# Optimization experiments

Hardware: AMD Instinct MI355X
Metric: run time of the kernel (lower is better)

## Reference

```python
import jax, jax.numpy as jnp
import numpy as np

N_NODES = 50000
N_GRAPHS = 500
BLOCK = N_NODES // N_GRAPHS  # 100 nodes per graph
N_EDGES = 800000
D = 32        # emb_dim = in_feat = out_feat
H = 4         # num_heads
R = 16        # num relations
N_CODES = 20000
L = 2         # n_layers
SLOPE = 0.2
LAM = 0.5     # loop_lambda


def setup_inputs() -> dict:
    key = jax.random.key(0)
    ks = jax.random.split(key, 20)
    node_ids = jax.random.randint(ks[0], (N_NODES,), 0, N_CODES)
    src = jax.random.randint(ks[1], (N_EDGES,), 0, N_NODES)
    # dst must live in the same graph as src (contiguous blocks of BLOCK nodes)
    off = jax.random.randint(ks[2], (N_EDGES,), 0, BLOCK)
    dst = (src // BLOCK) * BLOCK + off
    rel_type = jax.random.randint(ks[3], (N_EDGES,), 0, R)
    node2graph = jnp.repeat(jnp.arange(N_GRAPHS), BLOCK)
    state = jax.random.normal(ks[4], (N_GRAPHS, D), dtype=jnp.float32)
    readout_weight = jax.random.uniform(ks[5], (N_NODES,), dtype=jnp.float32)
    s = 1.0 / np.sqrt(D)
    code_emb = jax.random.uniform(ks[6], (N_CODES, D), minval=-1.0, maxval=1.0)
    rel_table = jax.random.uniform(ks[7], (R, D), minval=-1.0, maxval=1.0)
    W = jax.random.normal(ks[8], (L, R, D, D)) * s       # per-relation weights
    h_bias = jnp.zeros((L, D))
    Wr = jax.random.normal(ks[9], (L, D, H * D)) * s     # fc_rel_att
    br = jnp.zeros((L, H * D))
    We = jax.random.normal(ks[10], (L, D, H * D)) * s    # fc_edge_att
    be = jnp.zeros((L, H * D))
    attn_h = jax.random.normal(ks[11], (L, H, D)) * s
    attn_t = jax.random.normal(ks[12], (L, H, D)) * s
    attn_s = jax.random.normal(ks[13], (L, H, D)) * s
    attn_r = jax.random.normal(ks[14], (L, H, D)) * s
    attn_rs = jax.random.normal(ks[15], (L, H, D)) * s
    return dict(state=state, readout_weight=readout_weight, code_emb=code_emb,
                rel_table=rel_table, W=W, h_bias=h_bias, Wr=Wr, br=br, We=We, be=be,
                attn_h=attn_h, attn_t=attn_t, attn_s=attn_s, attn_r=attn_r, attn_rs=attn_rs,
                node_ids=node_ids, src=src, dst=dst, rel_type=rel_type, node2graph=node2graph)


def _forward(state, readout_weight, code_emb, rel_table, W, h_bias, Wr, br, We, be,
             attn_h, attn_t, attn_s, attn_r, attn_rs, node_ids, src, dst, rel_type, node2graph):
    lrelu = lambda x: jax.nn.leaky_relu(x, SLOPE)
    h = code_emb[node_ids]                      # [N, D]
    N = h.shape[0]
    G = state.shape[0]
    g_src = node2graph[src]                     # [E]
    rel_att = edge_att = None
    for l in range(L):
        # ---- relation attention (cal_rel_att, state path) ----
        rp = (rel_table @ Wr[l] + br[l]).reshape(R, H, D)
        sp = (state @ Wr[l] + br[l]).reshape(G, H, D)
        er = (rp * attn_r[l]).sum(-1)                       # [R, H]
        es = (sp * attn_rs[l]).sum(-1)                      # [G, H]
        ra = jax.nn.softmax(lrelu(er[None, :, :] + es[:, None, :]), axis=1)  # [G, R, H]
        rel_att = ra[g_src, rel_type]                       # [E, H]
        # ---- edge attention (cal_edge_att, state path) ----
        hp = (h @ We[l] + be[l]).reshape(N, H, D)           # multi-head src feat
        eh = (hp * attn_h[l]).sum(-1)                       # [N, H]
        et = (hp * attn_t[l]).sum(-1)                       # [N, H]
        nsp = (state[node2graph] @ We[l] + be[l]).reshape(N, H, D)
        esn = (nsp * attn_s[l]).sum(-1)                     # [N, H]
        e = lrelu(esn[src] + eh[src] + et[dst])             # [E, H]
        emax = jax.ops.segment_max(e, dst, num_segments=N)
        ex = jnp.exp(e - emax[dst])
        den = jax.ops.segment_sum(ex, dst, num_segments=N)
        edge_att = ex / den[dst]                            # edge_softmax over dst
        # ---- per-relation message: matmul(h_src, W[etype]) ----
        # transform all nodes per relation, then gather (same math as per-edge bmm)
        hW = jnp.einsum('nhd,rde->rnhe', hp, W[l])          # [R, N, H, D]
        msg = hW[rel_type, src]                             # [E, H, D]
        msg = (msg * edge_att[..., None] * rel_att[..., None]).sum(axis=1)  # [E, D]
        agg = jax.ops.segment_sum(msg, dst, num_segments=N) + h_bias[l]
        h = jax.nn.relu((1.0 - LAM) * agg + LAM * h)        # self-loop blend + relu
    x = jax.ops.segment_sum(h * readout_weight[:, None], node2graph, num_segments=G)
    return x, rel_att, edge_att


def reference(state, readout_weight, code_emb, rel_table, W, h_bias, Wr, br, We, be,
              attn_h, attn_t, attn_s, attn_r, attn_rs, node_ids, src, dst, rel_type, node2graph):
    return _forward(state, readout_weight, code_emb, rel_table, W, h_bias, Wr, br, We, be,
                    attn_h, attn_t, attn_s, attn_r, attn_rs, node_ids, src, dst, rel_type, node2graph)
```

## Files before the change

### kernel.cpp

```cpp
#include <hip/hip_runtime.h>
#include <hip/hip_fp16.h>

#define DI __device__ __forceinline__

constexpr int NGRAPH = 500;
constexpr int EDGES  = 800000;
constexpr int NNODE  = 50000;
constexpr int CAP    = 64;
constexpr int SCAT_BLOCKS = (EDGES + 255) / 256;

constexpr size_t WI_CURS  = 0;
constexpr size_t WI_SMETA = 50048;
constexpr size_t WF_PREP  = WI_SMETA + (size_t)NNODE * CAP;
constexpr size_t WF_WFRAG = WF_PREP + 672;
constexpr size_t WH_WC    = WF_WFRAG + 20480;

constexpr int S_H    = 0;
constexpr int S_HP   = 8000;
constexpr int S_U    = 33600;
constexpr int S_EH   = 136800;
constexpr int S_ET   = 138400;
constexpr int S_DEN  = 140000;
constexpr int S_RA   = 141600;
constexpr int S_ESG  = 141856;
constexpr int S_AH   = 141872;
constexpr int S_AT   = 142384;
constexpr int S_MLDS = 142896;
constexpr int S_RP   = 151088;
constexpr int S_TOTAL = 151496;
constexpr int UROW = 516;

typedef _Float16 f16x8 __attribute__((ext_vector_type(8)));
typedef _Float16 f16x2 __attribute__((ext_vector_type(2)));
typedef float f32x4 __attribute__((ext_vector_type(4)));

DI float lrelu(float x) { return x >= 0.f ? x : 0.2f * x; }
DI f16x8 u4_to_f16x8(uint4 u) { f16x8 r; __builtin_memcpy(&r, &u, 16); return r; }
DI f16x8 two_u2(uint2 a, uint2 b) { return u4_to_f16x8(make_uint4(a.x, a.y, b.x, b.y)); }
DI float h2f(unsigned short u) { __half hv; __builtin_memcpy(&hv, &u, 2); return __half2float(hv); }

DI float fdot2u(unsigned a, unsigned b, float c) {
    f16x2 av, bv;
    __builtin_memcpy(&av, &a, 4);
    __builtin_memcpy(&bv, &b, 4);
    return __builtin_amdgcn_fdot2(av, bv, c, false);
}

DI int hpIdx(int n, int c) { return n * 128 + (c ^ ((n & 7) << 3)); }

__global__ void k_prep(const int* __restrict__ src, const int* __restrict__ dst,
                       const int* __restrict__ rt, int* __restrict__ curs,
                       int* __restrict__ smeta,
                       const float* __restrict__ rel_table, const float* __restrict__ Wr,
                       const float* __restrict__ br, const float* __restrict__ We,
                       const float* __restrict__ be, const float* __restrict__ attn_r,
                       const float* __restrict__ attn_rs, const float* __restrict__ attn_s,
                       const float* __restrict__ W, float* __restrict__ prep,
                       uint4* __restrict__ wf) {
    __shared__ float wra[2][32][4];
    __shared__ float sbias[2][3][4];
    int bb = blockIdx.x, t = threadIdx.x;
    if (bb < SCAT_BLOCKS) {
        int e = bb * 256 + t;
        if (e >= EDGES) return;
        int s = src[e], d = dst[e], r = rt[e];
        int g = (unsigned)d / 100u;
        int pos = atomicAdd(&curs[d], 1);
        if (pos < CAP)
            smeta[((size_t)d << 6) + pos] = (s - g * 100) | (r << 7) | (e << 11);
        return;
    }
    int b = bb - SCAT_BLOCKS;
    if (b == 0) {
        {
            int l = t >> 7, k = (t >> 2) & 31, h = t & 3;
            float a = 0.f, b2 = 0.f, c = 0.f;
            for (int d2 = 0; d2 < 32; ++d2) {
                float w1 = Wr[(size_t)(l*32 + k)*128 + h*32 + d2];
                float w2 = We[(size_t)(l*32 + k)*128 + h*32 + d2];
                a  += w1 * attn_r [l*128 + h*32 + d2];
                b2 += w1 * attn_rs[l*128 + h*32 + d2];
                c  += w2 * attn_s [l*128 + h*32 + d2];
            }
            wra[l][k][h] = a;
            prep[128 + (l*32 + k)*4 + h] = b2;
            prep[384 + (l*32 + k)*4 + h] = c;
        }
        if (t < 24) {
            int l = t / 12, which = (t % 12) / 4, h = t % 4;
            const float* bp = (which == 2) ? be : br;
            const float* ap = (which == 0) ? attn_r : (which == 1 ? attn_rs : attn_s);
            float s = 0.f;
            for (int d2 = 0; d2 < 32; ++d2) s += bp[l*128 + h*32 + d2] * ap[l*128 + h*32 + d2];
            sbias[l][which][h] = s;
        }
        __syncthreads();
        if (t < 128) {
            int l = t >> 6, r = (t >> 2) & 15, h = t & 3;
            float s = sbias[l][0][h];
            for (int k = 0; k < 32; ++k) s += rel_table[r*32 + k] * wra[l][k][h];
            prep[(l*16 + r)*4 + h] = s;
        }
        if (t < 8) {
            int l = t >> 2, h = t & 3;
            prep[640 + l*4 + h] = sbias[l][1][h];
            prep[648 + l*4 + h] = sbias[l][2][h];
        }
    } else if (b <= 16) {
        int fi = (b - 1) * 256 + t;
        int ln = fi & 63, Nt = (fi >> 6) & 1, rel = (fi >> 7) & 15, l = fi >> 11;
        int j = Nt*16 + (ln & 15), k0 = (ln >> 4) << 3;
        unsigned short fr[8];
        #pragma unroll
        for (int i = 0; i < 8; ++i) {
            __half hv = __float2half(W[(((size_t)l*16 + rel)*32 + k0 + i)*32 + j]);
            __builtin_memcpy(&fr[i], &hv, 2);
        }
        uint4 o;
        o.x = fr[0] | ((unsigned)fr[1] << 16);
        o.y = fr[2] | ((unsigned)fr[3] << 16);
        o.z = fr[4] | ((unsigned)fr[5] << 16);
        o.w = fr[6] | ((unsigned)fr[7] << 16);
        wf[fi] = o;
    } else {
        int fi = (b - 17) * 256 + t;
        int ln = fi & 63, Nt = (fi >> 6) & 7, l = fi >> 9;
        int c = Nt*16 + (ln & 15);
        int phys = (c & 3)*32 + (c >> 2);
        int k0 = (ln >> 4) << 3;
        unsigned short fr[8];
        #pragma unroll
        for (int i = 0; i < 8; ++i) {
            __half hv = __float2half(We[(size_t)l*4096 + (k0 + i)*128 + phys]);
            __builtin_memcpy(&fr[i], &hv, 2);
        }
        uint4 o;
        o.x = fr[0] | ((unsigned)fr[1] << 16);
        o.y = fr[2] | ((unsigned)fr[3] << 16);
        o.z = fr[4] | ((unsigned)fr[5] << 16);
        o.w = fr[6] | ((unsigned)fr[7] << 16);
        wf[4096 + fi] = o;
    }
}

__global__ void __launch_bounds__(1024, 1)
k_fused(const float* __restrict__ state, const float* __restrict__ rw,
        const float* __restrict__ code_emb, const float* __restrict__ h_bias,
        const float* __restrict__ be, const float* __restrict__ attn_h,
        const float* __restrict__ attn_t, const int* __restrict__ node_ids,
        const int* __restrict__ curs, const int* __restrict__ smeta,
        const float* __restrict__ prep, const uint4* __restrict__ wf,
        unsigned short* __restrict__ wc,
        float* __restrict__ xout, float* __restrict__ relOut, float* __restrict__ edgeOut) {
    extern __shared__ char smem[];
    __half* hH  = (__half*)(smem + S_H);
    __half* hpH = (__half*)(smem + S_HP);
    __half* Uh  = (__half*)(smem + S_U);
    float* ehp  = (float*)(smem + S_EH);
    float* etp  = (float*)(smem + S_ET);
    float* denp = (float*)(smem + S_DEN);
    float* rap  = (float*)(smem + S_RA);
    float* esgp = (float*)(smem + S_ESG);
    float* sAH  = (float*)(smem + S_AH);
    float* sAT  = (float*)(smem + S_AT);
    int*   mlds = (int*)(smem + S_MLDS);
    int*   rp   = (int*)(smem + S_RP);
    const uint4* wfe = wf + 4096;

    const int g = blockIdx.x;
    const int t = threadIdx.x;
    const int lane = t & 63, w = t >> 6;
    const int ln15 = lane & 15, q = lane >> 4, q8 = q << 3;
    const int MtA = w % 7, NtA = w / 7;
    const bool hasT = (w < 14);
    const int cg = w >> 1;
    const int colc = cg * 16 + ln15;
    const int physc = (colc & 3) * 32 + (colc >> 2);
    const int Mt0 = (w & 1) ? 4 : 0;
    const int Mt1 = (w & 1) ? 7 : 4;

    unsigned short* wcg = wc + ((size_t)g << 13);
    const uint2* wcu = (const uint2*)wcg;

    for (int i = t; i < 1600; i += 1024) {
        int n = i >> 4, dp = i & 15;
        int id = node_ids[g * 100 + n];
        float2 v = *(const float2*)&code_emb[(size_t)id * 32 + dp * 2];
        *(__half2*)&hH[n * 40 + dp * 2] = __floats2half2_rn(v.x, v.y);
    }
    if (t < 100) { int c = curs[g * 100 + t]; rp[t + 1] = c < CAP ? c : CAP; }
    if (t == 0) rp[0] = 0;
    __syncthreads();
    for (int o = 1; o < 128; o <<= 1) {
        int v = 0;
        if (t <= 100 && t >= o) v = rp[t - o];
        __syncthreads();
        if (t <= 100 && t >= o) rp[t] += v;
        __syncthreads();
    }
    for (int i = t; i < 100 * CAP; i += 1024) {
        int bin = i >> 6, pos = i & 63;
        int lo = rp[bin], cnt = rp[bin + 1] - lo;
        if (pos < cnt)
            mlds[lo + pos] = smeta[(((size_t)(g * 100 + bin)) << 6) + pos];
    }

    for (int l = 0; l < 2; ++l) {
        __syncthreads();

        for (int i = t; i < 6450; i += 1024) ((uint4*)(smem + S_U))[i] = make_uint4(0, 0, 0, 0);
        if (t < 128) {
            sAH[t] = attn_h[l * 128 + (t & 3) * 32 + (t >> 2)];
            sAT[t] = attn_t[l * 128 + (t & 3) * 32 + (t >> 2)];
        }
        {
            uint4 bwe = wfe[(l * 8 + cg) * 64 + lane];
            f16x8 bw = u4_to_f16x8(bwe);
            float beC = be[l * 128 + physc];
            f32x4 z = {0.f, 0.f, 0.f, 0.f};
            for (int Mt = Mt0; Mt < Mt1; ++Mt) {
                const __half* hr = hH + (Mt * 16 + ln15) * 40 + q8;
                f32x4 pc = __builtin_amdgcn_mfma_f32_16x16x32_f16(
                    two_u2(*(const uint2*)hr, *(const uint2*)(hr + 4)), bw, z, 0, 0, 0);
                #pragma unroll
                for (int i = 0; i < 4; ++i) {
                    int n = Mt * 16 + q * 4 + i;
                    if (n < 100) hpH[hpIdx(n, colc)] = __float2half(pc[i] + beC);
                }
            }
        }
        {
            int k32 = lane & 31;
            float sG = state[g * 32 + k32];
            float4 frs = *(const float4*)&prep[128 + l * 128 + k32 * 4];
            float4 fes = *(const float4*)&prep[384 + l * 128 + k32 * 4];
            float p0 = sG * frs.x, p1 = sG * frs.y, p2 = sG * frs.z, p3 = sG * frs.w;
            float q0 = sG * fes.x, q1 = sG * fes.y, q2 = sG * fes.z, q3 = sG * fes.w;
            #pragma unroll
            for (int m = 1; m < 32; m <<= 1) {
                p0 += __shfl_xor(p0, m); p1 += __shfl_xor(p1, m);
                p2 += __shfl_xor(p2, m); p3 += __shfl_xor(p3, m);
                q0 += __shfl_xor(q0, m); q1 += __shfl_xor(q1, m);
                q2 += __shfl_xor(q2, m); q3 += __shfl_xor(q3, m);
            }
            int h = lane & 3;
            float esh  = (h & 2) ? ((h & 1) ? p3 : p2) : ((h & 1) ? p1 : p0);
            float esgh = (h & 2) ? ((h & 1) ? q3 : q2) : ((h & 1) ? q1 : q0);
            esh  += prep[640 + l * 4 + h];
            esgh += prep[648 + l * 4 + h];
            if (lane < 4) esgp[lane] = esgh;
            float er = prep[l * 64 + lane];
            float ex = __expf(lrelu(er + esh));
            float s = ex;
            s += __shfl_xor(s, 4); s += __shfl_xor(s, 8);
            s += __shfl_xor(s, 16); s += __shfl_xor(s, 32);
            rap[lane] = ex / s;
        }
        __syncthreads();

        if (t < 100) {
            int s = t;
            int sw = (s & 7) << 3;
            float eh[4] = {0, 0, 0, 0}, et[4] = {0, 0, 0, 0};
            #pragma unroll 4
            for (int i = 0; i < 16; ++i) {
                uint4 hv = *(const uint4*)&hpH[s * 128 + ((i * 8) ^ sw)];
                unsigned short hu[8];
                __builtin_memcpy(hu, &hv, 16);
                #pragma unroll
                for (int k = 0; k < 8; ++k) {
                    float f = h2f(hu[k]);
                    eh[k & 3] += f * sAH[i * 8 + k];
                    et[k & 3] += f * sAT[i * 8 + k];
                }
            }
            *(float4*)&ehp[s * 4] = make_float4(eh[0], eh[1], eh[2], eh[3]);
            *(float4*)&etp[s * 4] = make_float4(et[0], et[1], et[2], et[3]);
        }
        __syncthreads();

        if (t < 400) {
            int d = t >> 2, h = t & 3;
            int lo = rp[d], hi = rp[d + 1];
            float etd = etp[d * 4 + h] + esgp[h];
            float den = 0.f;
            for (int e = lo; e < hi; ++e) {
                int m = mlds[e];
                den += __expf(lrelu(ehp[(m & 127) * 4 + h] + etd));
            }
            denp[d * 4 + h] = den;
            float inv = 1.f / den;
            bool wAtt = (l == 1);
            for (int e = lo; e < hi; ++e) {
                int m = mlds[e];
                int r = (m >> 7) & 15;
                float a = __expf(lrelu(ehp[(m & 127) * 4 + h] + etd)) * inv;
                __half ch = __float2half(a * rap[r * 4 + h]);
                __builtin_memcpy(&wcg[e * 4 + h], &ch, 2);
                if (wAtt) {
                    int oe = (m >> 11) & 0xFFFFF;
                    edgeOut[(size_t)oe * 4 + h] = a;
                    relOut[(size_t)oe * 4 + h] = rap[r * 4 + h];
                }
            }
        }
        __syncthreads();

        if (t < 800) {
            int d = t >> 3, j = t & 7;
            int lo = rp[d], hi = rp[d + 1];
            for (int e = lo; e < hi; ++e) {
                int m = mlds[e];
                int s = m & 127, r = (m >> 7) & 15;
                uint2 cc = wcu[e];
                int sw = (s & 7) << 3;
                uint4 hv0 = *(const uint4*)&hpH[s * 128 + ((j * 16) ^ sw)];
                uint4 hv1 = *(const uint4*)&hpH[s * 128 + ((j * 16 + 8) ^ sw)];
                float v0 = fdot2u(cc.x, hv0.x, fdot2u(cc.y, hv0.y, 0.f));
                float v1 = fdot2u(cc.x, hv0.z, fdot2u(cc.y, hv0.w, 0.f));
                float v2 = fdot2u(cc.x, hv1.x, fdot2u(cc.y, hv1.y, 0.f));
                float v3 = fdot2u(cc.x, hv1.z, fdot2u(cc.y, hv1.w, 0.f));
                __half2 v01 = __floats2half2_rn(v0, v1);
                __half2 v23 = __floats2half2_rn(v2, v3);
                __half2* up = (__half2*)(Uh + d * UROW + r * 32 + j * 4);
                up[0] = __hadd2(up[0], v01);
                up[1] = __hadd2(up[1], v23);
            }
        }
        __syncthreads();

        f32x4 accA = {0.f, 0.f, 0.f, 0.f};
        if (hasT) {
            #pragma unroll 4
            for (int rel = 0; rel < 16; ++rel) {
                uint4 bAu = wf[((l * 16 + rel) * 2 + NtA) * 64 + lane];
                const __half* up = Uh + (MtA * 16 + ln15) * UROW + rel * 32 + q8;
                f16x8 af = two_u2(*(const uint2*)up, *(const uint2*)(up + 4));
                accA = __builtin_amdgcn_mfma_f32_16x16x32_f16(af, u4_to_f16x8(bAu), accA, 0, 0, 0);
            }
        }
        if (hasT) {
            int dcol = NtA * 16 + ln15;
            float bias = h_bias[l * 32 + dcol];
            #pragma unroll
            for (int i = 0; i < 4; ++i) {
                int n = MtA * 16 + q * 4 + i;
                if (n < 100) {
                    float hold = __half2float(hH[n * 40 + dcol]);
                    float hn = fmaxf(0.f, 0.5f * (accA[i] + bias) + 0.5f * hold);
                    hH[n * 40 + dcol] = __float2half(hn);
                }
            }
        }
    }
    __syncthreads();

    float* redp = (float*)(smem + S_U);
    {
        int part = t >> 5, d = t & 31;
        float acc = 0.f;
        for (int n = part; n < 100; n += 32)
            acc += __half2float(hH[n * 40 + d]) * rw[g * 100 + n];
        redp[part * 32 + d] = acc;
    }
    __syncthreads();
    if (t < 32) {
        float s = 0.f;
        #pragma unroll
        for (int p = 0; p < 32; ++p) s += redp[p * 32 + t];
        xout[g * 32 + t] = s;
    }
}

extern "C" void kernel_launch(void* const* d_in, const int* in_sizes, int n_in,
                              void* d_out, int out_size, void* d_ws, size_t ws_size,
                              hipStream_t stream) {
    const float* state     = (const float*)d_in[0];
    const float* rw        = (const float*)d_in[1];
    const float* code_emb  = (const float*)d_in[2];
    const float* rel_table = (const float*)d_in[3];
    const float* W         = (const float*)d_in[4];
    const float* h_bias    = (const float*)d_in[5];
    const float* Wr        = (const float*)d_in[6];
    const float* br        = (const float*)d_in[7];
    const float* We        = (const float*)d_in[8];
    const float* be        = (const float*)d_in[9];
    const float* attn_h    = (const float*)d_in[10];
    const float* attn_t    = (const float*)d_in[11];
    const float* attn_s    = (const float*)d_in[12];
    const float* attn_r    = (const float*)d_in[13];
    const float* attn_rs   = (const float*)d_in[14];
    const int* node_ids    = (const int*)d_in[15];
    const int* src         = (const int*)d_in[16];
    const int* dst         = (const int*)d_in[17];
    const int* rtype       = (const int*)d_in[18];

    float* out = (float*)d_out;
    float* xout = out;
    float* relOut = out + (size_t)NGRAPH * 32;
    float* edgeOut = relOut + (size_t)EDGES * 4;

    int* wsi = (int*)d_ws;
    float* wsf = (float*)d_ws;
    int* curs   = wsi + WI_CURS;
    int* smeta  = wsi + WI_SMETA;
    float* prep = wsf + WF_PREP;
    uint4* wfrag = (uint4*)(wsf + WF_WFRAG);
    unsigned short* wc = (unsigned short*)(wsf + WH_WC);

    (void)hipMemsetAsync(curs, 0, NNODE * sizeof(int), stream);
    k_prep<<<SCAT_BLOCKS + 21, 256, 0, stream>>>(src, dst, rtype, curs, smeta,
                                                 rel_table, Wr, br, We, be,
                                                 attn_r, attn_rs, attn_s, W, prep, wfrag);

    (void)hipFuncSetAttribute((const void*)k_fused, hipFuncAttributeMaxDynamicSharedMemorySize, S_TOTAL);
    k_fused<<<NGRAPH, 1024, S_TOTAL, stream>>>(state, rw, code_emb, h_bias, be,
                                               attn_h, attn_t, node_ids, curs, smeta,
                                               prep, wfrag, wc, xout, relOut, edgeOut);
}
```

Baseline: 169.0 us.

## Split edge-softmax denominator across more threads, cache exps, prefetch aggregation loop

Adds a separate phase where 800 threads each compute half of a destination/head edge range, storing unnormalised exponentials as fp16 in the per-graph coefficient buffer and partial denominators in shared memory. The normalisation phase then reads those cached values instead of recomputing exp twice. The attention-logit dot products switch to packed half2 FMAs with fp16 attention vectors. The message-aggregation loop software-prefetches the next edge's metadata and features. This costs an extra barrier and fp16 accumulation precision in the logits and stored exponentials.

```diff
diff --git a/kernel.cpp b/kernel.cpp
--- a/kernel.cpp
+++ b/kernel.cpp
@@ -20,14 +20,14 @@
 constexpr int S_U    = 33600;
 constexpr int S_EH   = 136800;
 constexpr int S_ET   = 138400;
-constexpr int S_DEN  = 140000;
 constexpr int S_RA   = 141600;
 constexpr int S_ESG  = 141856;
 constexpr int S_AH   = 141872;
 constexpr int S_AT   = 142384;
 constexpr int S_MLDS = 142896;
 constexpr int S_RP   = 151088;
-constexpr int S_TOTAL = 151496;
+constexpr int S_DEN2 = 151496;
+constexpr int S_TOTAL = S_DEN2 + 3200;
 constexpr int UROW = 516;
 
 typedef _Float16 f16x8 __attribute__((ext_vector_type(8)));
@@ -158,13 +158,13 @@
     __half* Uh  = (__half*)(smem + S_U);
     float* ehp  = (float*)(smem + S_EH);
     float* etp  = (float*)(smem + S_ET);
-    float* denp = (float*)(smem + S_DEN);
     float* rap  = (float*)(smem + S_RA);
     float* esgp = (float*)(smem + S_ESG);
-    float* sAH  = (float*)(smem + S_AH);
-    float* sAT  = (float*)(smem + S_AT);
+    __half* sAHh = (__half*)(smem + S_AH);
+    __half* sATh = (__half*)(smem + S_AT);
     int*   mlds = (int*)(smem + S_MLDS);
     int*   rp   = (int*)(smem + S_RP);
+    float* den2 = (float*)(smem + S_DEN2);
     const uint4* wfe = wf + 4096;
 
     const int g = blockIdx.x;
@@ -210,8 +210,8 @@
 
         for (int i = t; i < 6450; i += 1024) ((uint4*)(smem + S_U))[i] = make_uint4(0, 0, 0, 0);
         if (t < 128) {
-            sAH[t] = attn_h[l * 128 + (t & 3) * 32 + (t >> 2)];
-            sAT[t] = attn_t[l * 128 + (t & 3) * 32 + (t >> 2)];
+            sAHh[t] = __float2half(attn_h[l * 128 + (t & 3) * 32 + (t >> 2)]);
+            sATh[t] = __float2half(attn_t[l * 128 + (t & 3) * 32 + (t >> 2)]);
         }
         {
             uint4 bwe = wfe[(l * 8 + cg) * 64 + lane];
@@ -259,47 +259,68 @@
         __syncthreads();
 
         if (t < 100) {
-            int s = t;
-            int sw = (s & 7) << 3;
-            float eh[4] = {0, 0, 0, 0}, et[4] = {0, 0, 0, 0};
-            #pragma unroll 4
+            int s = t, sw = (s & 7) << 3;
+            __half2 eh01 = __floats2half2_rn(0.f, 0.f), eh23 = eh01;
+            __half2 et01 = eh01, et23 = eh01;
+            const __half2* ahp = (const __half2*)sAHh;
+            const __half2* atp = (const __half2*)sATh;
+            #pragma unroll
             for (int i = 0; i < 16; ++i) {
                 uint4 hv = *(const uint4*)&hpH[s * 128 + ((i * 8) ^ sw)];
-                unsigned short hu[8];
-                __builtin_memcpy(hu, &hv, 16);
-                #pragma unroll
-                for (int k = 0; k < 8; ++k) {
-                    float f = h2f(hu[k]);
-                    eh[k & 3] += f * sAH[i * 8 + k];
-                    et[k & 3] += f * sAT[i * 8 + k];
-                }
-            }
-            *(float4*)&ehp[s * 4] = make_float4(eh[0], eh[1], eh[2], eh[3]);
-            *(float4*)&etp[s * 4] = make_float4(et[0], et[1], et[2], et[3]);
+                __half2 a01 = *(__half2*)&hv.x, a23 = *(__half2*)&hv.y;
+                __half2 b01 = *(__half2*)&hv.z, b23 = *(__half2*)&hv.w;
+                eh01 = __hfma2(a01, ahp[i * 4 + 0], eh01);
+                eh23 = __hfma2(a23, ahp[i * 4 + 1], eh23);
+                eh01 = __hfma2(b01, ahp[i * 4 + 2], eh01);
+                eh23 = __hfma2(b23, ahp[i * 4 + 3], eh23);
+                et01 = __hfma2(a01, atp[i * 4 + 0], et01);
+                et23 = __hfma2(a23, atp[i * 4 + 1], et23);
+                et01 = __hfma2(b01, atp[i * 4 + 2], et01);
+                et23 = __hfma2(b23, atp[i * 4 + 3], et23);
+            }
+            float2 f01 = __half22float2(eh01), f23 = __half22float2(eh23);
+            *(float4*)&ehp[s * 4] = make_float4(f01.x, f01.y, f23.x, f23.y);
+            float2 g01 = __half22float2(et01), g23 = __half22float2(et23);
+            *(float4*)&etp[s * 4] = make_float4(g01.x, g01.y, g23.x, g23.y);
+        }
+        __syncthreads();
+
+        if (t < 800) {
+            int d = t >> 3, h = (t >> 1) & 3, half = t & 1;
+            int lo0 = rp[d], hi0 = rp[d + 1];
+            int mid = (lo0 + hi0 + 1) >> 1;
+            int lo = half ? mid : lo0, hi = half ? hi0 : mid;
+            float etd = etp[d * 4 + h] + esgp[h];
+            float den = 0.f;
+            int m = (lo < hi) ? mlds[lo] : 0;
+            float ev = (lo < hi) ? ehp[(m & 127) * 4 + h] : 0.f;
+            for (int e = lo; e < hi; ++e) {
+                int m2 = 0; float ev2 = 0.f;
+                if (e + 1 < hi) { m2 = mlds[e + 1]; ev2 = ehp[(m2 & 127) * 4 + h]; }
+                float x = __expf(lrelu(ev + etd));
+                __half ch = __float2half(x);
+                __builtin_memcpy(&wcg[e * 4 + h], &ch, 2);
+                den += x;
+                m = m2; ev = ev2;
+            }
+            den2[t] = den;
         }
         __syncthreads();
 
         if (t < 400) {
             int d = t >> 2, h = t & 3;
             int lo = rp[d], hi = rp[d + 1];
-            float etd = etp[d * 4 + h] + esgp[h];
-            float den = 0.f;
-            for (int e = lo; e < hi; ++e) {
-                int m = mlds[e];
-                den += __expf(lrelu(ehp[(m & 127) * 4 + h] + etd));
-            }
-            denp[d * 4 + h] = den;
+            float den = den2[d * 8 + h * 2] + den2[d * 8 + h * 2 + 1];
             float inv = 1.f / den;
-            bool wAtt = (l == 1);
             for (int e = lo; e < hi; ++e) {
                 int m = mlds[e];
                 int r = (m >> 7) & 15;
-                float a = __expf(lrelu(ehp[(m & 127) * 4 + h] + etd)) * inv;
-                __half ch = __float2half(a * rap[r * 4 + h]);
+                float x = h2f(wcg[e * 4 + h]) * inv;
+                __half ch = __float2half(x * rap[r * 4 + h]);
                 __builtin_memcpy(&wcg[e * 4 + h], &ch, 2);
-                if (wAtt) {
+                if (l == 1) {
                     int oe = (m >> 11) & 0xFFFFF;
-                    edgeOut[(size_t)oe * 4 + h] = a;
+                    edgeOut[(size_t)oe * 4 + h] = x;
                     relOut[(size_t)oe * 4 + h] = rap[r * 4 + h];
                 }
             }
@@ -309,22 +330,35 @@
         if (t < 800) {
             int d = t >> 3, j = t & 7;
             int lo = rp[d], hi = rp[d + 1];
-            for (int e = lo; e < hi; ++e) {
-                int m = mlds[e];
-                int s = m & 127, r = (m >> 7) & 15;
-                uint2 cc = wcu[e];
-                int sw = (s & 7) << 3;
-                uint4 hv0 = *(const uint4*)&hpH[s * 128 + ((j * 16) ^ sw)];
-                uint4 hv1 = *(const uint4*)&hpH[s * 128 + ((j * 16 + 8) ^ sw)];
-                float v0 = fdot2u(cc.x, hv0.x, fdot2u(cc.y, hv0.y, 0.f));
-                float v1 = fdot2u(cc.x, hv0.z, fdot2u(cc.y, hv0.w, 0.f));
-                float v2 = fdot2u(cc.x, hv1.x, fdot2u(cc.y, hv1.y, 0.f));
-                float v3 = fdot2u(cc.x, hv1.z, fdot2u(cc.y, hv1.w, 0.f));
-                __half2 v01 = __floats2half2_rn(v0, v1);
-                __half2 v23 = __floats2half2_rn(v2, v3);
-                __half2* up = (__half2*)(Uh + d * UROW + r * 32 + j * 4);
-                up[0] = __hadd2(up[0], v01);
-                up[1] = __hadd2(up[1], v23);
+            if (lo < hi) {
+                int m = mlds[lo];
+                uint2 cc = wcu[lo];
+                int s0 = m & 127, sw0 = (s0 & 7) << 3;
+                uint4 hv0 = *(const uint4*)&hpH[s0 * 128 + ((j * 16) ^ sw0)];
+                uint4 hv1 = *(const uint4*)&hpH[s0 * 128 + ((j * 16 + 8) ^ sw0)];
+                for (int e = lo; e < hi; ++e) {
+                    int m2 = 0;
+                    uint2 cc2 = make_uint2(0, 0);
+                    uint4 nv0 = make_uint4(0, 0, 0, 0), nv1 = nv0;
+                    if (e + 1 < hi) {
+                        m2 = mlds[e + 1];
+                        cc2 = wcu[e + 1];
+                        int s2 = m2 & 127, sw2 = (s2 & 7) << 3;
+                        nv0 = *(const uint4*)&hpH[s2 * 128 + ((j * 16) ^ sw2)];
+                        nv1 = *(const uint4*)&hpH[s2 * 128 + ((j * 16 + 8) ^ sw2)];
+                    }
+                    int r = (m >> 7) & 15;
+                    float v0 = fdot2u(cc.x, hv0.x, fdot2u(cc.y, hv0.y, 0.f));
+                    float v1 = fdot2u(cc.x, hv0.z, fdot2u(cc.y, hv0.w, 0.f));
+                    float v2 = fdot2u(cc.x, hv1.x, fdot2u(cc.y, hv1.y, 0.f));
+                    float v3 = fdot2u(cc.x, hv1.z, fdot2u(cc.y, hv1.w, 0.f));
+                    __half2 v01 = __floats2half2_rn(v0, v1);
+                    __half2 v23 = __floats2half2_rn(v2, v3);
+                    __half2* up = (__half2*)(Uh + d * UROW + r * 32 + j * 4);
+                    up[0] = __hadd2(up[0], v01);
+                    up[1] = __hadd2(up[1], v23);
+                    m = m2; cc = cc2; hv0 = nv0; hv1 = nv1;
+                }
             }
         }
         __syncthreads();
```

Result: slower. 175.1 us (+3.6%).

## Split relation scatter into four passes to shrink LDS and raise occupancy

Applied to the files above, without the earlier changes.

The per-graph U buffer now holds only 4 relations at a time instead of 16, so the relation loop runs in four passes of scatter then MFMA. This cuts LDS from about 151KB to about 72KB and halves the block size to 512 threads, so more than one block can sit on a CU. Waves pick up a second MFMA tile, and the attention vectors are stored as half. The cost is four scans over each node's edge list with skipped edges, plus extra barriers and zeroing per pass, and less parallelism inside each block.

```diff
diff --git a/kernel.cpp b/kernel.cpp
--- a/kernel.cpp
+++ b/kernel.cpp
@@ -18,17 +18,16 @@
 constexpr int S_H    = 0;
 constexpr int S_HP   = 8000;
 constexpr int S_U    = 33600;
-constexpr int S_EH   = 136800;
-constexpr int S_ET   = 138400;
-constexpr int S_DEN  = 140000;
-constexpr int S_RA   = 141600;
-constexpr int S_ESG  = 141856;
-constexpr int S_AH   = 141872;
-constexpr int S_AT   = 142384;
-constexpr int S_MLDS = 142896;
-constexpr int S_RP   = 151088;
-constexpr int S_TOTAL = 151496;
-constexpr int UROW = 516;
+constexpr int S_EH   = 60000;
+constexpr int S_ET   = 61600;
+constexpr int S_RA   = 63200;
+constexpr int S_ESG  = 63456;
+constexpr int S_AH   = 63472;
+constexpr int S_AT   = 63728;
+constexpr int S_MLDS = 63984;
+constexpr int S_RP   = 72176;
+constexpr int S_TOTAL = 72584;
+constexpr int UROW = 132;
 
 typedef _Float16 f16x8 __attribute__((ext_vector_type(8)));
 typedef _Float16 f16x2 __attribute__((ext_vector_type(2)));
@@ -143,7 +142,7 @@
     }
 }
 
-__global__ void __launch_bounds__(1024, 1)
+__global__ void __launch_bounds__(512, 4)
 k_fused(const float* __restrict__ state, const float* __restrict__ rw,
         const float* __restrict__ code_emb, const float* __restrict__ h_bias,
         const float* __restrict__ be, const float* __restrict__ attn_h,
@@ -158,11 +157,10 @@
     __half* Uh  = (__half*)(smem + S_U);
     float* ehp  = (float*)(smem + S_EH);
     float* etp  = (float*)(smem + S_ET);
-    float* denp = (float*)(smem + S_DEN);
     float* rap  = (float*)(smem + S_RA);
     float* esgp = (float*)(smem + S_ESG);
-    float* sAH  = (float*)(smem + S_AH);
-    float* sAT  = (float*)(smem + S_AT);
+    __half* sAHh = (__half*)(smem + S_AH);
+    __half* sATh = (__half*)(smem + S_AT);
     int*   mlds = (int*)(smem + S_MLDS);
     int*   rp   = (int*)(smem + S_RP);
     const uint4* wfe = wf + 4096;
@@ -172,17 +170,15 @@
     const int lane = t & 63, w = t >> 6;
     const int ln15 = lane & 15, q = lane >> 4, q8 = q << 3;
     const int MtA = w % 7, NtA = w / 7;
-    const bool hasT = (w < 14);
-    const int cg = w >> 1;
-    const int colc = cg * 16 + ln15;
+    const int MtB = (w + 8) % 7, NtB = (w + 8) / 7;
+    const bool hasB = (w < 6);
+    const int colc = w * 16 + ln15;
     const int physc = (colc & 3) * 32 + (colc >> 2);
-    const int Mt0 = (w & 1) ? 4 : 0;
-    const int Mt1 = (w & 1) ? 7 : 4;
 
     unsigned short* wcg = wc + ((size_t)g << 13);
     const uint2* wcu = (const uint2*)wcg;
 
-    for (int i = t; i < 1600; i += 1024) {
+    for (int i = t; i < 1600; i += 512) {
         int n = i >> 4, dp = i & 15;
         int id = node_ids[g * 100 + n];
         float2 v = *(const float2*)&code_emb[(size_t)id * 32 + dp * 2];
@@ -198,7 +194,7 @@
         if (t <= 100 && t >= o) rp[t] += v;
         __syncthreads();
     }
-    for (int i = t; i < 100 * CAP; i += 1024) {
+    for (int i = t; i < 100 * CAP; i += 512) {
         int bin = i >> 6, pos = i & 63;
         int lo = rp[bin], cnt = rp[bin + 1] - lo;
         if (pos < cnt)
@@ -208,17 +204,16 @@
     for (int l = 0; l < 2; ++l) {
         __syncthreads();
 
-        for (int i = t; i < 6450; i += 1024) ((uint4*)(smem + S_U))[i] = make_uint4(0, 0, 0, 0);
         if (t < 128) {
-            sAH[t] = attn_h[l * 128 + (t & 3) * 32 + (t >> 2)];
-            sAT[t] = attn_t[l * 128 + (t & 3) * 32 + (t >> 2)];
+            sAHh[t] = __float2half(attn_h[l * 128 + (t & 3) * 32 + (t >> 2)]);
+            sATh[t] = __float2half(attn_t[l * 128 + (t & 3) * 32 + (t >> 2)]);
         }
         {
-            uint4 bwe = wfe[(l * 8 + cg) * 64 + lane];
+            uint4 bwe = wfe[(l * 8 + w) * 64 + lane];
             f16x8 bw = u4_to_f16x8(bwe);
             float beC = be[l * 128 + physc];
             f32x4 z = {0.f, 0.f, 0.f, 0.f};
-            for (int Mt = Mt0; Mt < Mt1; ++Mt) {
+            for (int Mt = 0; Mt < 7; ++Mt) {
                 const __half* hr = hH + (Mt * 16 + ln15) * 40 + q8;
                 f32x4 pc = __builtin_amdgcn_mfma_f32_16x16x32_f16(
                     two_u2(*(const uint2*)hr, *(const uint2*)(hr + 4)), bw, z, 0, 0, 0);
@@ -270,8 +265,8 @@
                 #pragma unroll
                 for (int k = 0; k < 8; ++k) {
                     float f = h2f(hu[k]);
-                    eh[k & 3] += f * sAH[i * 8 + k];
-                    et[k & 3] += f * sAT[i * 8 + k];
+                    eh[k & 3] += f * __half2float(sAHh[i * 8 + k]);
+                    et[k & 3] += f * __half2float(sATh[i * 8 + k]);
                 }
             }
             *(float4*)&ehp[s * 4] = make_float4(eh[0], eh[1], eh[2], eh[3]);
@@ -288,7 +283,6 @@
                 int m = mlds[e];
                 den += __expf(lrelu(ehp[(m & 127) * 4 + h] + etd));
             }
-            denp[d * 4 + h] = den;
             float inv = 1.f / den;
             bool wAtt = (l == 1);
             for (int e = lo; e < hi; ++e) {
@@ -306,40 +300,63 @@
         }
         __syncthreads();
 
-        if (t < 800) {
-            int d = t >> 3, j = t & 7;
-            int lo = rp[d], hi = rp[d + 1];
-            for (int e = lo; e < hi; ++e) {
-                int m = mlds[e];
-                int s = m & 127, r = (m >> 7) & 15;
-                uint2 cc = wcu[e];
-                int sw = (s & 7) << 3;
-                uint4 hv0 = *(const uint4*)&hpH[s * 128 + ((j * 16) ^ sw)];
-                uint4 hv1 = *(const uint4*)&hpH[s * 128 + ((j * 16 + 8) ^ sw)];
-                float v0 = fdot2u(cc.x, hv0.x, fdot2u(cc.y, hv0.y, 0.f));
-                float v1 = fdot2u(cc.x, hv0.z, fdot2u(cc.y, hv0.w, 0.f));
-                float v2 = fdot2u(cc.x, hv1.x, fdot2u(cc.y, hv1.y, 0.f));
-                float v3 = fdot2u(cc.x, hv1.z, fdot2u(cc.y, hv1.w, 0.f));
-                __half2 v01 = __floats2half2_rn(v0, v1);
-                __half2 v23 = __floats2half2_rn(v2, v3);
-                __half2* up = (__half2*)(Uh + d * UROW + r * 32 + j * 4);
-                up[0] = __hadd2(up[0], v01);
-                up[1] = __hadd2(up[1], v23);
-            }
-        }
-        __syncthreads();
-
         f32x4 accA = {0.f, 0.f, 0.f, 0.f};
-        if (hasT) {
-            #pragma unroll 4
-            for (int rel = 0; rel < 16; ++rel) {
-                uint4 bAu = wf[((l * 16 + rel) * 2 + NtA) * 64 + lane];
-                const __half* up = Uh + (MtA * 16 + ln15) * UROW + rel * 32 + q8;
-                f16x8 af = two_u2(*(const uint2*)up, *(const uint2*)(up + 4));
-                accA = __builtin_amdgcn_mfma_f32_16x16x32_f16(af, u4_to_f16x8(bAu), accA, 0, 0, 0);
-            }
-        }
-        if (hasT) {
+        f32x4 accB = {0.f, 0.f, 0.f, 0.f};
+        for (int p = 0; p < 4; ++p) {
+            for (int i = t; i < 1650; i += 512) ((uint4*)(smem + S_U))[i] = make_uint4(0, 0, 0, 0);
+            __syncthreads();
+
+            if (t < 400) {
+                int d = t >> 2, j = t & 3;
+                int lo = rp[d], hi = rp[d + 1];
+                for (int e = lo; e < hi; ++e) {
+                    int m = mlds[e];
+                    int r = (m >> 7) & 15;
+                    if ((r >> 2) != p) continue;
+                    int s = m & 127;
+                    uint2 cc = wcu[e];
+                    int sw = (s & 7) << 3;
+                    uint4 hv0 = *(const uint4*)&hpH[s * 128 + ((j * 32) ^ sw)];
+                    uint4 hv1 = *(const uint4*)&hpH[s * 128 + ((j * 32 + 8) ^ sw)];
+                    uint4 hv2 = *(const uint4*)&hpH[s * 128 + ((j * 32 + 16) ^ sw)];
+                    uint4 hv3 = *(const uint4*)&hpH[s * 128 + ((j * 32 + 24) ^ sw)];
+                    float v0 = fdot2u(cc.x, hv0.x, fdot2u(cc.y, hv0.y, 0.f));
+                    float v1 = fdot2u(cc.x, hv0.z, fdot2u(cc.y, hv0.w, 0.f));
+                    float v2 = fdot2u(cc.x, hv1.x, fdot2u(cc.y, hv1.y, 0.f));
+                    float v3 = fdot2u(cc.x, hv1.z, fdot2u(cc.y, hv1.w, 0.f));
+                    float v4 = fdot2u(cc.x, hv2.x, fdot2u(cc.y, hv2.y, 0.f));
+                    float v5 = fdot2u(cc.x, hv2.z, fdot2u(cc.y, hv2.w, 0.f));
+                    float v6 = fdot2u(cc.x, hv3.x, fdot2u(cc.y, hv3.y, 0.f));
+                    float v7 = fdot2u(cc.x, hv3.z, fdot2u(cc.y, hv3.w, 0.f));
+                    __half2* up = (__half2*)(Uh + d * UROW + (r & 3) * 32 + j * 8);
+                    up[0] = __hadd2(up[0], __floats2half2_rn(v0, v1));
+                    up[1] = __hadd2(up[1], __floats2half2_rn(v2, v3));
+                    up[2] = __hadd2(up[2], __floats2half2_rn(v4, v5));
+                    up[3] = __hadd2(up[3], __floats2half2_rn(v6, v7));
+                }
+            }
+            __syncthreads();
+
+            #pragma unroll
+            for (int kq = 0; kq < 4; ++kq) {
+                int rel = p * 4 + kq;
+                {
+                    uint4 bAu = wf[((l * 16 + rel) * 2 + NtA) * 64 + lane];
+                    const __half* up = Uh + (MtA * 16 + ln15) * UROW + kq * 32 + q8;
+                    f16x8 af = two_u2(*(const uint2*)up, *(const uint2*)(up + 4));
+                    accA = __builtin_amdgcn_mfma_f32_16x16x32_f16(af, u4_to_f16x8(bAu), accA, 0, 0, 0);
+                }
+                if (hasB) {
+                    uint4 bBu = wf[((l * 16 + rel) * 2 + NtB) * 64 + lane];
+                    const __half* up = Uh + (MtB * 16 + ln15) * UROW + kq * 32 + q8;
+                    f16x8 af = two_u2(*(const uint2*)up, *(const uint2*)(up + 4));
+                    accB = __builtin_amdgcn_mfma_f32_16x16x32_f16(af, u4_to_f16x8(bBu), accB, 0, 0, 0);
+                }
+            }
+            __syncthreads();
+        }
+
+        {
             int dcol = NtA * 16 + ln15;
             float bias = h_bias[l * 32 + dcol];
             #pragma unroll
@@ -352,6 +369,19 @@
                 }
             }
         }
+        if (hasB) {
+            int dcol = NtB * 16 + ln15;
+            float bias = h_bias[l * 32 + dcol];
+            #pragma unroll
+            for (int i = 0; i < 4; ++i) {
+                int n = MtB * 16 + q * 4 + i;
+                if (n < 100) {
+                    float hold = __half2float(hH[n * 40 + dcol]);
+                    float hn = fmaxf(0.f, 0.5f * (accB[i] + bias) + 0.5f * hold);
+                    hH[n * 40 + dcol] = __float2half(hn);
+                }
+            }
+        }
     }
     __syncthreads();
 
@@ -359,7 +389,7 @@
     {
         int part = t >> 5, d = t & 31;
         float acc = 0.f;
-        for (int n = part; n < 100; n += 32)
+        for (int n = part; n < 100; n += 16)
             acc += __half2float(hH[n * 40 + d]) * rw[g * 100 + n];
         redp[part * 32 + d] = acc;
     }
@@ -367,7 +397,7 @@
     if (t < 32) {
         float s = 0.f;
         #pragma unroll
-        for (int p = 0; p < 32; ++p) s += redp[p * 32 + t];
+        for (int p = 0; p < 16; ++p) s += redp[p * 32 + t];
         xout[g * 32 + t] = s;
     }
 }
@@ -414,7 +444,7 @@
                                                  attn_r, attn_rs, attn_s, W, prep, wfrag);
 
     (void)hipFuncSetAttribute((const void*)k_fused, hipFuncAttributeMaxDynamicSharedMemorySize, S_TOTAL);
-    k_fused<<<NGRAPH, 1024, S_TOTAL, stream>>>(state, rw, code_emb, h_bias, be,
-                                               attn_h, attn_t, node_ids, curs, smeta,
-                                               prep, wfrag, wc, xout, relOut, edgeOut);
+    k_fused<<<NGRAPH, 512, S_TOTAL, stream>>>(state, rw, code_emb, h_bias, be,
+                                              attn_h, attn_t, node_ids, curs, smeta,
+                                              prep, wfrag, wc, xout, relOut, edgeOut);
 }
```

Measured after the change: 193.1 us. +14.3%, slower.
